# Kernel optimization log

Hardware: AMD Instinct MI355X
Metric: run time of the kernel (lower is better)

## Reference

```python
import jax, jax.numpy as jnp
import numpy as np

N, D, E = 100000, 128, 600000  # nodes, channels, edges per subgraph


def _cos(a, b, eps=1e-8):
    # torch.nn.functional.cosine_similarity semantics (norm clamped at eps)
    na = jnp.maximum(jnp.linalg.norm(a, axis=-1), eps)
    nb = jnp.maximum(jnp.linalg.norm(b, axis=-1), eps)
    return jnp.sum(a * b, axis=-1) / (na * nb)


def _get_edge_att(x, edge_index, edge_attr):
    # utils.get_edge_att (source unavailable): edge weight modulated by
    # endpoint-feature cosine similarity.
    return edge_attr * _cos(x[edge_index[0]], x[edge_index[1]])


def _cgat(x, edge_index, edge_attr, node_mask, W, b):
    m = node_mask[:, None]
    h = jnp.where(m, x @ W.T, x)                       # lin only on masked nodes
    msg = edge_attr[:, None] * h[edge_index[0]]        # [E, D]
    ssum = jax.ops.segment_sum(msg, edge_index[1], num_segments=N)
    cnt = jax.ops.segment_sum(jnp.ones_like(edge_attr), edge_index[1], num_segments=N)
    mean = ssum / jnp.maximum(cnt, 1.0)[:, None]       # safe mean (0 for isolated nodes)
    out = jnp.where(m, mean, 0.0) + h                  # aggr only written at masked nodes
    return jnp.where(m, jax.nn.sigmoid(out + b), out)


def setup_inputs() -> dict:
    key = jax.random.key(0)
    ks = jax.random.split(key, 10)
    x = jax.random.normal(ks[0], (N, D), jnp.float32)
    edge_index_ii = jax.random.randint(ks[1], (2, E), 0, N)
    edge_attr_ii = jax.random.uniform(ks[2], (E,), jnp.float32)
    edge_index_uiu = jax.random.randint(ks[3], (2, E), 0, N)
    edge_attr_uiu = jax.random.uniform(ks[4], (E,), jnp.float32)
    node_mask_item = jnp.arange(N) < (N * 8 // 10)
    s = 1.0 / np.sqrt(D)  # torch Linear default init range
    W1_ii = jax.random.uniform(ks[5], (D, D), jnp.float32, -s, s)
    W2_ii = jax.random.uniform(ks[6], (D, D), jnp.float32, -s, s)
    W_uiu = jax.random.uniform(ks[7], (D, D), jnp.float32, -s, s)
    z = jnp.zeros((D,), jnp.float32)  # bias zero-initialized in reset_parameters
    return {
        "x": x,
        "edge_attr_ii": edge_attr_ii,
        "edge_attr_uiu": edge_attr_uiu,
        "W1_ii": W1_ii, "b1_ii": z, "W2_ii": W2_ii, "b2_ii": z,
        "W_uiu": W_uiu, "b_uiu": z,
        "edge_index_ii": edge_index_ii,
        "edge_index_uiu": edge_index_uiu,
        "node_mask_item": node_mask_item,
    }


def reference(x, edge_attr_ii, edge_attr_uiu, W1_ii, b1_ii, W2_ii, b2_ii,
              W_uiu, b_uiu, edge_index_ii, edge_index_uiu, node_mask_item):
    # item-item graph
    ea1 = _get_edge_att(x, edge_index_ii, edge_attr_ii)
    x1 = _cgat(x, edge_index_ii, ea1, node_mask_item, W1_ii, b1_ii)
    ea2 = _get_edge_att(x1, edge_index_ii, edge_attr_ii)
    x2 = _cgat(x1, edge_index_ii, ea2, node_mask_item, W2_ii, b2_ii)
    # user-item graph (cgat1_uiu applied twice in the source)
    all_mask = jnp.ones((N,), bool)
    u1 = _cgat(x2, edge_index_uiu, edge_attr_uiu, all_mask, W_uiu, b_uiu)
    u2 = _cgat(u1, edge_index_uiu, edge_attr_uiu, all_mask, W_uiu, b_uiu)
    # edge predictions on the uiu edges (the only nonzero part of edge_y_pred)
    return _cos(u2[edge_index_uiu[0]], u2[edge_index_uiu[1]])
```

## Files before the change

### kernel.cpp

```cpp
#include <hip/hip_runtime.h>
#include <cstdint>
#include <cmath>

#define D 128
#define SCAN_BS 1024

typedef __attribute__((ext_vector_type(8))) short bf16x8;
typedef __attribute__((ext_vector_type(4))) float f32x4;

__device__ __forceinline__ unsigned short f2b(float f) {
    unsigned u = __float_as_uint(f);
    return (unsigned short)((u + 0x7FFFu + ((u >> 16) & 1u)) >> 16);
}
__device__ __forceinline__ unsigned pack2(float a, float b) {
    return (unsigned)f2b(a) | ((unsigned)f2b(b) << 16);
}
__device__ __forceinline__ float blo(unsigned u) { return __uint_as_float(u << 16); }
__device__ __forceinline__ float bhi(unsigned u) { return __uint_as_float(u & 0xffff0000u); }
__device__ __forceinline__ int swzbyte(int row, int b) {
    return (row << 8) + (b ^ ((row & 7) << 4));
}

__global__ void mask_canon_kernel(const unsigned char* __restrict__ mraw,
                                  int* __restrict__ mout, int n) {
    int i = blockIdx.x * blockDim.x + threadIdx.x;
    if (i >= n) return;
    bool isbool = (mraw[1] | mraw[2] | mraw[3]) != 0;
    int v;
    if (isbool) v = (mraw[i] != 0);
    else        v = (((const int*)mraw)[i] != 0);
    mout[i] = v;
}

__global__ void conv_norm_kernel(const float* __restrict__ x,
                                 unsigned short* __restrict__ xb,
                                 unsigned short* __restrict__ xnb, int n) {
    int t = blockIdx.x * blockDim.x + threadIdx.x;
    int i = t >> 4, sl = t & 15;
    if (i >= n) return;
    unsigned rid = ((unsigned)i << 4) | (unsigned)sl;
    const float4* ip = (const float4*)(x + (size_t)i * D) + sl * 2;
    float4 a = ip[0], b = ip[1];
    float f[8] = {a.x, a.y, a.z, a.w, b.x, b.y, b.z, b.w};
    float acc = 0.f;
    #pragma unroll
    for (int q = 0; q < 8; q++) acc += f[q] * f[q];
    #pragma unroll
    for (int o = 8; o; o >>= 1) acc += __shfl_xor(acc, o);
    float r = 1.0f / fmaxf(sqrtf(acc), 1e-8f);
    uint4 ob, on;
    #pragma unroll
    for (int q = 0; q < 4; q++) {
        (&ob.x)[q] = pack2(f[2*q], f[2*q+1]);
        (&on.x)[q] = pack2(f[2*q] * r, f[2*q+1] * r);
    }
    ((uint4*)xb)[rid] = ob;
    ((uint4*)xnb)[rid] = on;
}

__global__ void w3_to_b16_kernel(const float* __restrict__ W1, const float* __restrict__ W2,
                                 const float* __restrict__ Wu,
                                 unsigned short* __restrict__ o1, unsigned short* __restrict__ o2,
                                 unsigned short* __restrict__ ou) {
    int t = blockIdx.x * blockDim.x + threadIdx.x;
    const float* src; unsigned short* dst; int b;
    if (t < 2048)      { src = W1; dst = o1; b = t; }
    else if (t < 4096) { src = W2; dst = o2; b = t - 2048; }
    else               { src = Wu; dst = ou; b = t - 4096; }
    const float4* ip = (const float4*)src + (size_t)b * 2;
    float4 a = ip[0], c = ip[1];
    uint4 o;
    o.x = pack2(a.x, a.y); o.y = pack2(a.z, a.w);
    o.z = pack2(c.x, c.y); o.w = pack2(c.z, c.w);
    ((uint4*)dst)[b] = o;
}

__global__ void count_pos2_kernel(const int* __restrict__ dstA, const int* __restrict__ dstB,
                                  int* __restrict__ tmp2, int* __restrict__ posw,
                                  int n, int e_total) {
    int t = blockIdx.x * blockDim.x + threadIdx.x;
    if (t >= 2 * e_total) return;
    int g = (t >= e_total);
    int e = t - g * e_total;
    int d = (g ? dstB : dstA)[e];
    posw[t] = atomicAdd(&tmp2[(size_t)g * n + d], 1);
}

__global__ __launch_bounds__(SCAN_BS)
void scan_block_kernel(const int* __restrict__ deg2, int* __restrict__ off2,
                       int* __restrict__ bsum2, int n) {
    __shared__ int s[SCAN_BS];
    int g = blockIdx.y;
    int gid = blockIdx.x * SCAN_BS + threadIdx.x;
    int v = (gid < n) ? deg2[(size_t)g * n + gid] : 0;
    s[threadIdx.x] = v;
    __syncthreads();
    for (int o = 1; o < SCAN_BS; o <<= 1) {
        int t = (threadIdx.x >= o) ? s[threadIdx.x - o] : 0;
        __syncthreads();
        s[threadIdx.x] += t;
        __syncthreads();
    }
    if (gid < n) off2[(size_t)g * (n + 1) + gid] = s[threadIdx.x] - v;
    if (threadIdx.x == SCAN_BS - 1) bsum2[g * 256 + blockIdx.x] = s[SCAN_BS - 1];
}

__global__ void scan_bsum_kernel(int* __restrict__ bsum2, int nb) {
    __shared__ int s[256];
    int g = blockIdx.y;
    int v = ((int)threadIdx.x < nb) ? bsum2[g * 256 + threadIdx.x] : 0;
    s[threadIdx.x] = v;
    __syncthreads();
    for (int o = 1; o < 256; o <<= 1) {
        int t = (threadIdx.x >= o) ? s[threadIdx.x - o] : 0;
        __syncthreads();
        s[threadIdx.x] += t;
        __syncthreads();
    }
    if ((int)threadIdx.x < nb) bsum2[g * 256 + threadIdx.x] = s[threadIdx.x] - v;
}

__global__ __launch_bounds__(SCAN_BS)
void add_offsets_kernel(int* __restrict__ off2, const int* __restrict__ bsum2,
                        int n, int e_total) {
    int g = blockIdx.y;
    int gid = blockIdx.x * SCAN_BS + threadIdx.x;
    if (gid < n) off2[(size_t)g * (n + 1) + gid] += bsum2[g * 256 + blockIdx.x];
    if (gid == 0) off2[(size_t)g * (n + 1) + n] = e_total;
}

__global__ void scatter_edges2_kernel(const int* __restrict__ srcA, const int* __restrict__ dstA,
                                      const float* __restrict__ aA,
                                      const int* __restrict__ srcB, const int* __restrict__ dstB,
                                      const float* __restrict__ aB,
                                      const int* __restrict__ off2, const int* __restrict__ posw,
                                      int2* __restrict__ edaA, int2* __restrict__ edaB,
                                      int n, int e_total) {
    int t = blockIdx.x * blockDim.x + threadIdx.x;
    if (t >= 2 * e_total) return;
    int g = (t >= e_total);
    int e = t - g * e_total;
    int d = (g ? dstB : dstA)[e];
    int p = off2[(size_t)g * (n + 1) + d] + posw[t];
    int2 rec;
    rec.x = (g ? srcB : srcA)[e];
    rec.y = __float_as_int((g ? aB : aA)[e]);
    (g ? edaB : edaA)[p] = rec;
}

__global__ __launch_bounds__(512)
void gemm_mfma_kernel(const unsigned short* __restrict__ xb,
                      const unsigned short* __restrict__ Wb,
                      const int* __restrict__ mask,
                      unsigned short* __restrict__ hb, int n) {
    __shared__ char sXb[128 * 256];
    __shared__ char sWb[128 * 256];
    const int tid = threadIdx.x;
    const int blockRow0 = blockIdx.x * 128;

    const uint4* xg = (const uint4*)xb + (size_t)blockRow0 * 16;
    #pragma unroll
    for (int it = 0; it < 4; it++) {
        int f = tid + it * 512;
        int row = f >> 4, kc = f & 15;
        uint4 v = make_uint4(0, 0, 0, 0);
        if (blockRow0 + row < n) v = xg[f];
        *(uint4*)(sXb + swzbyte(row, kc * 16)) = v;
    }
    const uint4* wg = (const uint4*)Wb;
    #pragma unroll
    for (int it = 0; it < 4; it++) {
        int f = tid + it * 512;
        int row = f >> 4, kc = f & 15;
        *(uint4*)(sWb + swzbyte(row, kc * 16)) = wg[f];
    }
    __syncthreads();

    const int wid = tid >> 6, lane = tid & 63;
    const int lrow = lane & 15, kg = lane >> 4;
    f32x4 acc[8];
    #pragma unroll
    for (int j = 0; j < 8; j++) acc[j] = (f32x4)(0.f);

    const int arow = wid * 16 + lrow;
    #pragma unroll
    for (int kk = 0; kk < 4; kk++) {
        int kb = kk * 64 + kg * 16;
        bf16x8 af = *(const bf16x8*)(sXb + swzbyte(arow, kb));
        #pragma unroll
        for (int j = 0; j < 8; j++) {
            bf16x8 bfr = *(const bf16x8*)(sWb + swzbyte(j * 16 + lrow, kb));
            acc[j] = __builtin_amdgcn_mfma_f32_16x16x32_bf16(af, bfr, acc[j], 0, 0, 0);
        }
    }

    const int growbase = blockRow0 + wid * 16 + kg * 4;
    const int lrbase = wid * 16 + kg * 4;
    #pragma unroll
    for (int r = 0; r < 4; r++) {
        int row = growbase + r;
        if (row >= n) continue;
        bool pm = mask ? (mask[row] != 0) : true;
        int lr = lrbase + r;
        #pragma unroll
        for (int j = 0; j < 8; j++) {
            int col = j * 16 + lrow;
            unsigned short o;
            if (pm) o = f2b(acc[j][r]);
            else    o = *(const unsigned short*)(sXb + (lr << 8) + ((2 * col) ^ ((lr & 7) << 4)));
            hb[(size_t)row * D + col] = o;
        }
    }
}

__global__ __launch_bounds__(256)
void fused_agg_kernel(const unsigned short* __restrict__ hb,
                      const unsigned short* __restrict__ xnb,
                      const int2* __restrict__ eda,
                      const int* __restrict__ off,
                      const float* __restrict__ bias, const int* __restrict__ mask,
                      unsigned short* __restrict__ outb,
                      unsigned short* __restrict__ xnout, int n) {
    int t = blockIdx.x * blockDim.x + threadIdx.x;
    int i = t >> 4, sl = t & 15;
    if (i >= n) return;
    const uint4* h4 = (const uint4*)hb;
    const uint4* x4 = (const uint4*)xnb;
    uint4* o4 = (uint4*)outb;
    unsigned rid = ((unsigned)i << 4) | (unsigned)sl;
    uint4 hv = h4[rid];
    bool m = mask ? (mask[i] != 0) : true;

    float fo[8];
    if (!m) {
        #pragma unroll
        for (int q = 0; q < 4; q++) {
            unsigned u = (&hv.x)[q];
            fo[2*q] = blo(u); fo[2*q+1] = bhi(u);
        }
    } else {
        float xd[8];
        if (xnb) {
            uint4 xv = x4[rid];
            #pragma unroll
            for (int q = 0; q < 4; q++) {
                unsigned u = (&xv.x)[q];
                xd[2*q] = blo(u); xd[2*q+1] = bhi(u);
            }
        }

        int s0 = off[i], s1 = off[i + 1];
        float acc[8];
        #pragma unroll
        for (int k = 0; k < 8; k++) acc[k] = 0.f;

        int p = s0;
        for (; p + 2 <= s1; p += 2) {
            int2 e0 = eda[p], e1 = eda[p + 1];
            unsigned r0 = ((unsigned)e0.x << 4) | (unsigned)sl;
            unsigned r1 = ((unsigned)e1.x << 4) | (unsigned)sl;
            uint4 h0 = h4[r0], h1 = h4[r1];
            float c0 = __int_as_float(e0.y), c1 = __int_as_float(e1.y);
            if (xnb) {
                uint4 x0 = x4[r0], x1 = x4[r1];
                float pr0 = 0.f, pr1 = 0.f;
                #pragma unroll
                for (int q = 0; q < 4; q++) {
                    unsigned u0 = (&x0.x)[q], u1 = (&x1.x)[q];
                    pr0 += blo(u0) * xd[2*q] + bhi(u0) * xd[2*q+1];
                    pr1 += blo(u1) * xd[2*q] + bhi(u1) * xd[2*q+1];
                }
                #pragma unroll
                for (int o = 8; o; o >>= 1) {
                    pr0 += __shfl_xor(pr0, o);
                    pr1 += __shfl_xor(pr1, o);
                }
                c0 *= pr0; c1 *= pr1;
            }
            #pragma unroll
            for (int q = 0; q < 4; q++) {
                unsigned u0 = (&h0.x)[q], u1 = (&h1.x)[q];
                acc[2*q]   += c0 * blo(u0) + c1 * blo(u1);
                acc[2*q+1] += c0 * bhi(u0) + c1 * bhi(u1);
            }
        }
        if (p < s1) {
            int2 e0 = eda[p];
            unsigned r0 = ((unsigned)e0.x << 4) | (unsigned)sl;
            uint4 h0 = h4[r0];
            float c0 = __int_as_float(e0.y);
            if (xnb) {
                uint4 x0 = x4[r0];
                float pr0 = 0.f;
                #pragma unroll
                for (int q = 0; q < 4; q++) {
                    unsigned u0 = (&x0.x)[q];
                    pr0 += blo(u0) * xd[2*q] + bhi(u0) * xd[2*q+1];
                }
                #pragma unroll
                for (int o = 8; o; o >>= 1) pr0 += __shfl_xor(pr0, o);
                c0 *= pr0;
            }
            #pragma unroll
            for (int q = 0; q < 4; q++) {
                unsigned u0 = (&h0.x)[q];
                acc[2*q]   += c0 * blo(u0);
                acc[2*q+1] += c0 * bhi(u0);
            }
        }

        float inv = 1.0f / fmaxf((float)(s1 - s0), 1.0f);
        const float4* bp = (const float4*)(bias + 8 * sl);
        float4 bv0 = bp[0], bv1 = bp[1];
        float bb[8] = {bv0.x, bv0.y, bv0.z, bv0.w, bv1.x, bv1.y, bv1.z, bv1.w};
        #pragma unroll
        for (int q = 0; q < 4; q++) {
            unsigned u = (&hv.x)[q];
            float z0 = acc[2*q]   * inv + blo(u) + bb[2*q];
            float z1 = acc[2*q+1] * inv + bhi(u) + bb[2*q+1];
            fo[2*q]   = 1.0f / (1.0f + __expf(-z0));
            fo[2*q+1] = 1.0f / (1.0f + __expf(-z1));
        }
    }

    uint4 o;
    #pragma unroll
    for (int q = 0; q < 4; q++) (&o.x)[q] = pack2(fo[2*q], fo[2*q+1]);
    o4[rid] = o;

    if (xnout) {
        float ss = 0.f;
        #pragma unroll
        for (int k = 0; k < 8; k++) ss += fo[k] * fo[k];
        #pragma unroll
        for (int o2 = 8; o2; o2 >>= 1) ss += __shfl_xor(ss, o2);
        float r = 1.0f / fmaxf(sqrtf(ss), 1e-8f);
        uint4 on;
        #pragma unroll
        for (int q = 0; q < 4; q++) (&on.x)[q] = pack2(fo[2*q] * r, fo[2*q+1] * r);
        ((uint4*)xnout)[rid] = on;
    }
}

__global__ void edge_cos_b16_kernel(const unsigned short* __restrict__ xb,
                                    const int* __restrict__ src,
                                    const int* __restrict__ dst,
                                    float* __restrict__ out, int e_total) {
    int t = blockIdx.x * blockDim.x + threadIdx.x;
    int e = t >> 4, lane = t & 15;
    if (e >= e_total) return;
    int s = src[e], d = dst[e];
    uint4 a = ((const uint4*)xb)[((unsigned)s << 4) | lane];
    uint4 b = ((const uint4*)xb)[((unsigned)d << 4) | lane];
    float sd = 0.f, ss = 0.f, dd = 0.f;
    #pragma unroll
    for (int q = 0; q < 4; q++) {
        unsigned ua = (&a.x)[q], ub = (&b.x)[q];
        float a0 = blo(ua), a1 = bhi(ua), b0 = blo(ub), b1 = bhi(ub);
        sd += a0 * b0 + a1 * b1;
        ss += a0 * a0 + a1 * a1;
        dd += b0 * b0 + b1 * b1;
    }
    #pragma unroll
    for (int o = 8; o; o >>= 1) {
        sd += __shfl_xor(sd, o, 16);
        ss += __shfl_xor(ss, o, 16);
        dd += __shfl_xor(dd, o, 16);
    }
    if (lane == 0) {
        float rs = 1.0f / fmaxf(sqrtf(ss), 1e-8f);
        float rd = 1.0f / fmaxf(sqrtf(dd), 1e-8f);
        out[e] = sd * rs * rd;
    }
}

extern "C" void kernel_launch(void* const* d_in, const int* in_sizes, int n_in,
                              void* d_out, int out_size, void* d_ws, size_t ws_size,
                              hipStream_t stream) {
    const float* x        = (const float*)d_in[0];
    const float* attr_ii  = (const float*)d_in[1];
    const float* attr_uiu = (const float*)d_in[2];
    const float* W1       = (const float*)d_in[3];
    const float* b1       = (const float*)d_in[4];
    const float* W2       = (const float*)d_in[5];
    const float* b2       = (const float*)d_in[6];
    const float* Wu       = (const float*)d_in[7];
    const float* bu       = (const float*)d_in[8];
    const int*   ei_ii    = (const int*)d_in[9];
    const int*   ei_uiu   = (const int*)d_in[10];
    const unsigned char* mraw = (const unsigned char*)d_in[11];

    const int n = in_sizes[0] / D;
    const int e = in_sizes[1];
    const size_t ND = (size_t)n * D;

    unsigned short* Ab  = (unsigned short*)d_ws;
    unsigned short* Bb0 = Ab + ND;
    unsigned short* Bb1 = Bb0 + ND;
    unsigned short* Xn0 = Bb1 + ND;
    unsigned short* Xn1 = Xn0 + ND;
    unsigned short* Wb1 = Xn1 + ND;
    unsigned short* Wb2 = Wb1 + 16384;
    unsigned short* Wbu = Wb2 + 16384;
    int2* eda_ii  = (int2*)(Wbu + 16384);
    int2* eda_uiu = eda_ii + e;
    int* maskI    = (int*)(eda_uiu + e);
    int* tmp2     = maskI + n;
    int* bsum2    = tmp2 + 2 * (size_t)n;
    int* off2     = bsum2 + 512;
    int* off_ii   = off2;
    int* off_uiu  = off2 + (n + 1);
    int* posw     = (int*)Ab;

    const int* src_ii  = ei_ii,  * dst_ii  = ei_ii + e;
    const int* src_uiu = ei_uiu, * dst_uiu = ei_uiu + e;
    float* out = (float*)d_out;

    const int nb = (n + SCAN_BS - 1) / SCAN_BS;
    const int gN16 = ((size_t)n * 16 + 255) / 256;
    const int gE16 = ((size_t)e * 16 + 255) / 256;
    const int gGemm = (n + 127) / 128;

    mask_canon_kernel<<<(n + 255) / 256, 256, 0, stream>>>(mraw, maskI, n);

    hipMemsetAsync(tmp2, 0, 2 * (size_t)n * sizeof(int), stream);
    count_pos2_kernel<<<(2 * e + 255) / 256, 256, 0, stream>>>(dst_ii, dst_uiu, tmp2, posw, n, e);
    scan_block_kernel<<<dim3(nb, 2), SCAN_BS, 0, stream>>>(tmp2, off2, bsum2, n);
    scan_bsum_kernel<<<dim3(1, 2), 256, 0, stream>>>(bsum2, nb);
    add_offsets_kernel<<<dim3(nb, 2), SCAN_BS, 0, stream>>>(off2, bsum2, n, e);
    scatter_edges2_kernel<<<(2 * e + 255) / 256, 256, 0, stream>>>(
        src_ii, dst_ii, attr_ii, src_uiu, dst_uiu, attr_uiu, off2, posw, eda_ii, eda_uiu, n, e);

    conv_norm_kernel<<<gN16, 256, 0, stream>>>(x, Bb0, Xn0, n);
    w3_to_b16_kernel<<<24, 256, 0, stream>>>(W1, W2, Wu, Wb1, Wb2, Wbu);

    gemm_mfma_kernel<<<gGemm, 512, 0, stream>>>(Bb0, Wb1, maskI, Ab, n);
    fused_agg_kernel<<<gN16, 256, 0, stream>>>(Ab, Xn0, eda_ii, off_ii, b1, maskI, Bb1, Xn1, n);

    gemm_mfma_kernel<<<gGemm, 512, 0, stream>>>(Bb1, Wb2, maskI, Ab, n);
    fused_agg_kernel<<<gN16, 256, 0, stream>>>(Ab, Xn1, eda_ii, off_ii, b2, maskI, Bb0, nullptr, n);

    gemm_mfma_kernel<<<gGemm, 512, 0, stream>>>(Bb0, Wbu, nullptr, Ab, n);
    fused_agg_kernel<<<gN16, 256, 0, stream>>>(Ab, nullptr, eda_uiu, off_uiu, bu, nullptr, Bb1, nullptr, n);

    gemm_mfma_kernel<<<gGemm, 512, 0, stream>>>(Bb1, Wbu, nullptr, Ab, n);
    fused_agg_kernel<<<gN16, 256, 0, stream>>>(Ab, nullptr, eda_uiu, off_uiu, bu, nullptr, Bb0, nullptr, n);

    edge_cos_b16_kernel<<<gE16, 256, 0, stream>>>(Bb0, src_uiu, dst_uiu, out, e);
}
```

Before: 378.8 us.

## Sort nodes by in-degree for aggregation load balance and unroll edge loop by four

Builds a per-graph permutation of nodes bucketed by in-degree, with unmasked item nodes in their own bucket, using a histogram, scan and scatter. The aggregation kernel then processes nodes in that order, so the 16-lane groups in a wavefront have similar edge counts and the masked/unmasked branch is uniform. The edge loop is also unrolled from two to four edges to keep more gathers in flight. This adds three small preprocessing kernels, an extra perm lookup, and a scattered output write order that loses spatial locality.

Result: slower. 1.327 ms (+250.3%).

```diff
diff --git a/kernel.cpp b/kernel.cpp
--- a/kernel.cpp
+++ b/kernel.cpp
@@ -148,6 +148,48 @@
     (g ? edaB : edaA)[p] = rec;
 }
 
+__global__ void deg_hist_kernel(const int* __restrict__ tmp2, const int* __restrict__ maskI,
+                                int* __restrict__ dhist, int n) {
+    int t = blockIdx.x * blockDim.x + threadIdx.x;
+    if (t >= 2 * n) return;
+    int g = (t >= n);
+    int i = t - g * n;
+    int d = tmp2[t]; if (d > 62) d = 62;
+    int key = (!g && !maskI[i]) ? 63 : d;
+    atomicAdd(&dhist[g * 64 + key], 1);
+}
+
+__global__ void deg_scan_kernel(const int* __restrict__ dhist, int* __restrict__ dbase,
+                                int* __restrict__ dcnt) {
+    __shared__ int s[128];
+    int tid = threadIdx.x;
+    int v = dhist[tid];
+    s[tid] = v;
+    __syncthreads();
+    int seg = tid & 63;
+    for (int o = 1; o < 64; o <<= 1) {
+        int t = (seg >= o) ? s[tid - o] : 0;
+        __syncthreads();
+        s[tid] += t;
+        __syncthreads();
+    }
+    dbase[tid] = s[tid] - v;
+    dcnt[tid] = 0;
+}
+
+__global__ void deg_scatter_kernel(const int* __restrict__ tmp2, const int* __restrict__ maskI,
+                                   const int* __restrict__ dbase, int* __restrict__ dcnt,
+                                   int* __restrict__ perm, int n) {
+    int t = blockIdx.x * blockDim.x + threadIdx.x;
+    if (t >= 2 * n) return;
+    int g = (t >= n);
+    int i = t - g * n;
+    int d = tmp2[t]; if (d > 62) d = 62;
+    int key = (!g && !maskI[i]) ? 63 : d;
+    int p = dbase[g * 64 + key] + atomicAdd(&dcnt[g * 64 + key], 1);
+    perm[(size_t)g * n + p] = i;
+}
+
 __global__ __launch_bounds__(512)
 void gemm_mfma_kernel(const unsigned short* __restrict__ xb,
                       const unsigned short* __restrict__ Wb,
@@ -218,12 +260,14 @@
                       const unsigned short* __restrict__ xnb,
                       const int2* __restrict__ eda,
                       const int* __restrict__ off,
+                      const int* __restrict__ perm,
                       const float* __restrict__ bias, const int* __restrict__ mask,
                       unsigned short* __restrict__ outb,
                       unsigned short* __restrict__ xnout, int n) {
     int t = blockIdx.x * blockDim.x + threadIdx.x;
-    int i = t >> 4, sl = t & 15;
-    if (i >= n) return;
+    int il = t >> 4, sl = t & 15;
+    if (il >= n) return;
+    int i = perm[il];
     const uint4* h4 = (const uint4*)hb;
     const uint4* x4 = (const uint4*)xnb;
     uint4* o4 = (uint4*)outb;
@@ -255,8 +299,45 @@
         for (int k = 0; k < 8; k++) acc[k] = 0.f;
 
         int p = s0;
-        for (; p + 2 <= s1; p += 2) {
-            int2 e0 = eda[p], e1 = eda[p + 1];
+        while (p + 4 <= s1) {
+            int2 e0 = eda[p], e1 = eda[p+1], e2 = eda[p+2], e3 = eda[p+3];
+            unsigned r0 = ((unsigned)e0.x << 4) | (unsigned)sl;
+            unsigned r1 = ((unsigned)e1.x << 4) | (unsigned)sl;
+            unsigned r2 = ((unsigned)e2.x << 4) | (unsigned)sl;
+            unsigned r3 = ((unsigned)e3.x << 4) | (unsigned)sl;
+            uint4 h0 = h4[r0], h1 = h4[r1], h2 = h4[r2], h3 = h4[r3];
+            float c0 = __int_as_float(e0.y), c1 = __int_as_float(e1.y);
+            float c2 = __int_as_float(e2.y), c3 = __int_as_float(e3.y);
+            if (xnb) {
+                uint4 x0 = x4[r0], x1 = x4[r1], x2 = x4[r2], x3 = x4[r3];
+                float pr0 = 0.f, pr1 = 0.f, pr2 = 0.f, pr3 = 0.f;
+                #pragma unroll
+                for (int q = 0; q < 4; q++) {
+                    unsigned u0 = (&x0.x)[q], u1 = (&x1.x)[q], u2 = (&x2.x)[q], u3 = (&x3.x)[q];
+                    pr0 += blo(u0) * xd[2*q] + bhi(u0) * xd[2*q+1];
+                    pr1 += blo(u1) * xd[2*q] + bhi(u1) * xd[2*q+1];
+                    pr2 += blo(u2) * xd[2*q] + bhi(u2) * xd[2*q+1];
+                    pr3 += blo(u3) * xd[2*q] + bhi(u3) * xd[2*q+1];
+                }
+                #pragma unroll
+                for (int o = 8; o; o >>= 1) {
+                    pr0 += __shfl_xor(pr0, o);
+                    pr1 += __shfl_xor(pr1, o);
+                    pr2 += __shfl_xor(pr2, o);
+                    pr3 += __shfl_xor(pr3, o);
+                }
+                c0 *= pr0; c1 *= pr1; c2 *= pr2; c3 *= pr3;
+            }
+            #pragma unroll
+            for (int q = 0; q < 4; q++) {
+                unsigned u0 = (&h0.x)[q], u1 = (&h1.x)[q], u2 = (&h2.x)[q], u3 = (&h3.x)[q];
+                acc[2*q]   += c0 * blo(u0) + c1 * blo(u1) + c2 * blo(u2) + c3 * blo(u3);
+                acc[2*q+1] += c0 * bhi(u0) + c1 * bhi(u1) + c2 * bhi(u2) + c3 * bhi(u3);
+            }
+            p += 4;
+        }
+        if (p + 2 <= s1) {
+            int2 e0 = eda[p], e1 = eda[p+1];
             unsigned r0 = ((unsigned)e0.x << 4) | (unsigned)sl;
             unsigned r1 = ((unsigned)e1.x << 4) | (unsigned)sl;
             uint4 h0 = h4[r0], h1 = h4[r1];
@@ -283,6 +364,7 @@
                 acc[2*q]   += c0 * blo(u0) + c1 * blo(u1);
                 acc[2*q+1] += c0 * bhi(u0) + c1 * bhi(u1);
             }
+            p += 2;
         }
         if (p < s1) {
             int2 e0 = eda[p];
@@ -406,10 +488,16 @@
     int2* eda_uiu = eda_ii + e;
     int* maskI    = (int*)(eda_uiu + e);
     int* tmp2     = maskI + n;
-    int* bsum2    = tmp2 + 2 * (size_t)n;
+    int* dhist    = tmp2 + 2 * (size_t)n;
+    int* dcnt     = dhist + 128;
+    int* dbase    = dcnt + 128;
+    int* bsum2    = dbase + 128;
     int* off2     = bsum2 + 512;
     int* off_ii   = off2;
     int* off_uiu  = off2 + (n + 1);
+    int* perm2    = off2 + 2 * (n + 1);
+    int* perm_ii  = perm2;
+    int* perm_uiu = perm2 + n;
     int* posw     = (int*)Ab;
 
     const int* src_ii  = ei_ii,  * dst_ii  = ei_ii + e;
@@ -423,7 +511,7 @@
 
     mask_canon_kernel<<<(n + 255) / 256, 256, 0, stream>>>(mraw, maskI, n);
 
-    hipMemsetAsync(tmp2, 0, 2 * (size_t)n * sizeof(int), stream);
+    hipMemsetAsync(tmp2, 0, (2 * (size_t)n + 128) * sizeof(int), stream);
     count_pos2_kernel<<<(2 * e + 255) / 256, 256, 0, stream>>>(dst_ii, dst_uiu, tmp2, posw, n, e);
     scan_block_kernel<<<dim3(nb, 2), SCAN_BS, 0, stream>>>(tmp2, off2, bsum2, n);
     scan_bsum_kernel<<<dim3(1, 2), 256, 0, stream>>>(bsum2, nb);
@@ -431,20 +519,24 @@
     scatter_edges2_kernel<<<(2 * e + 255) / 256, 256, 0, stream>>>(
         src_ii, dst_ii, attr_ii, src_uiu, dst_uiu, attr_uiu, off2, posw, eda_ii, eda_uiu, n, e);
 
+    deg_hist_kernel<<<(2 * n + 255) / 256, 256, 0, stream>>>(tmp2, maskI, dhist, n);
+    deg_scan_kernel<<<1, 128, 0, stream>>>(dhist, dbase, dcnt);
+    deg_scatter_kernel<<<(2 * n + 255) / 256, 256, 0, stream>>>(tmp2, maskI, dbase, dcnt, perm2, n);
+
     conv_norm_kernel<<<gN16, 256, 0, stream>>>(x, Bb0, Xn0, n);
     w3_to_b16_kernel<<<24, 256, 0, stream>>>(W1, W2, Wu, Wb1, Wb2, Wbu);
 
     gemm_mfma_kernel<<<gGemm, 512, 0, stream>>>(Bb0, Wb1, maskI, Ab, n);
-    fused_agg_kernel<<<gN16, 256, 0, stream>>>(Ab, Xn0, eda_ii, off_ii, b1, maskI, Bb1, Xn1, n);
+    fused_agg_kernel<<<gN16, 256, 0, stream>>>(Ab, Xn0, eda_ii, off_ii, perm_ii, b1, maskI, Bb1, Xn1, n);
 
     gemm_mfma_kernel<<<gGemm, 512, 0, stream>>>(Bb1, Wb2, maskI, Ab, n);
-    fused_agg_kernel<<<gN16, 256, 0, stream>>>(Ab, Xn1, eda_ii, off_ii, b2, maskI, Bb0, nullptr, n);
+    fused_agg_kernel<<<gN16, 256, 0, stream>>>(Ab, Xn1, eda_ii, off_ii, perm_ii, b2, maskI, Bb0, nullptr, n);
 
     gemm_mfma_kernel<<<gGemm, 512, 0, stream>>>(Bb0, Wbu, nullptr, Ab, n);
-    fused_agg_kernel<<<gN16, 256, 0, stream>>>(Ab, nullptr, eda_uiu, off_uiu, bu, nullptr, Bb1, nullptr, n);
+    fused_agg_kernel<<<gN16, 256, 0, stream>>>(Ab, nullptr, eda_uiu, off_uiu, perm_uiu, bu, nullptr, Bb1, nullptr, n);
 
     gemm_mfma_kernel<<<gGemm, 512, 0, stream>>>(Bb1, Wbu, nullptr, Ab, n);
-    fused_agg_kernel<<<gN16, 256, 0, stream>>>(Ab, nullptr, eda_uiu, off_uiu, bu, nullptr, Bb0, nullptr, n);
+    fused_agg_kernel<<<gN16, 256, 0, stream>>>(Ab, nullptr, eda_uiu, off_uiu, perm_uiu, bu, nullptr, Bb0, nullptr, n);
 
     edge_cos_b16_kernel<<<gE16, 256, 0, stream>>>(Bb0, src_uiu, dst_uiu, out, e);
 }
```
